# Optimization experiments

Measured on AMD Instinct MI355X. Metric: run time of the kernel, lower is better.

The kernel has to match this reference:

```python
import jax, jax.numpy as jnp
import numpy as np

EPS = 1e-5

def _bn_relu(h, gamma, beta):
    # h: (b, c, n); BatchNorm1d in training mode: stats over (batch, spatial)
    mean = jnp.mean(h, axis=(0, 2), keepdims=True)
    var = jnp.var(h, axis=(0, 2), keepdims=True)
    h = (h - mean) * jax.lax.rsqrt(var + EPS)
    h = h * gamma[None, :, None] + beta[None, :, None]
    return jax.nn.relu(h)

def setup_inputs() -> dict:
    key = jax.random.key(0)
    ks = jax.random.split(key, 8)
    b, c, n, k, N = 4, 128, 4096, 32, 16384
    x = jax.random.normal(ks[0], (b, c, n, k), dtype=jnp.float32)
    group_idx = jax.random.randint(ks[1], (b, n, k), 0, N, dtype=jnp.int64)
    fps_idx = jax.random.randint(ks[2], (b, n), 0, N, dtype=jnp.int64)
    w1 = jax.random.normal(ks[3], (c, 2 * c), dtype=jnp.float32) * (1.0 / np.sqrt(2 * c))
    b1 = jnp.zeros((c,), dtype=jnp.float32)
    g1 = jnp.ones((c,), dtype=jnp.float32)
    be1 = jnp.zeros((c,), dtype=jnp.float32)
    w2 = jax.random.normal(ks[4], (c, c), dtype=jnp.float32) * (1.0 / np.sqrt(c))
    b2 = jnp.zeros((c,), dtype=jnp.float32)
    g2 = jnp.ones((c,), dtype=jnp.float32)
    be2 = jnp.zeros((c,), dtype=jnp.float32)
    return {"x": x, "group_idx": group_idx, "fps_idx": fps_idx, "N": N,
            "w1": w1, "b1": b1, "g1": g1, "be1": be1,
            "w2": w2, "b2": b2, "g2": g2, "be2": be2}

def reference(x, group_idx, fps_idx, N, w1, b1, g1, be1, w2, b2, g2, be2):
    b, c, n, k = x.shape
    # local max pool over neighbors: (b, c, n)
    group_x = jnp.max(x, axis=-1)
    # scatter_max of (b, n*k, c) into (b, N, c), out initialized to zeros
    dil = jnp.transpose(x, (0, 2, 3, 1)).reshape(b * n * k, c)
    idx = group_idx.reshape(b, n * k) + (jnp.arange(b, dtype=group_idx.dtype) * N)[:, None]
    seg = jax.ops.segment_max(dil, idx.reshape(-1), num_segments=b * N)
    # torch scatter_max with zero-initialized out: max with 0, empty segs -> 0
    seg = jnp.maximum(seg, 0.0).reshape(b, N, c)
    # gather FPS-sampled points: (b, n, c) -> (b, c, n)
    gathered = jnp.take_along_axis(seg, fps_idx[:, :, None], axis=1)
    dilated_x = jnp.transpose(gathered, (0, 2, 1))
    feat = jnp.concatenate([group_x, dilated_x], axis=1)  # (b, 2c, n)
    h = jnp.einsum('oc,bcn->bon', w1, feat) + b1[None, :, None]
    h = _bn_relu(h, g1, be1)
    h = jnp.einsum('oc,bcn->bon', w2, h) + b2[None, :, None]
    h = _bn_relu(h, g2, be2)
    return h
```

## Files before the change

### kernel.cpp

```cpp
#include <hip/hip_runtime.h>

constexpr int Bb = 4, Cc = 128, Nn = 4096, Kk = 32, Ns = 16384;
constexpr int ROWS = Bb * Nn;
constexpr int NK = Nn * Kk;
constexpr float EPS = 1e-5f;

constexpr size_t SZ_SEG   = (size_t)Bb * Ns * Cc * 4;
constexpr size_t OFF_SEG  = 0;
constexpr size_t SZ_GX    = (size_t)ROWS * Cc * 4;
constexpr size_t OFF_GX   = OFF_SEG + SZ_SEG;
constexpr size_t OFF_H1   = OFF_GX + SZ_GX;
constexpr size_t OFF_H2   = OFF_H1 + SZ_GX;
constexpr size_t SZ_PART  = (size_t)256 * 128 * 2 * 4;
constexpr size_t OFF_P1   = OFF_H2 + SZ_GX;
constexpr size_t OFF_P2   = OFF_P1 + SZ_PART;
constexpr size_t OFF_FLAG = OFF_P2 + SZ_PART;

__global__ __launch_bounds__(256) void k_prep(const int* __restrict__ fps,
                                              float4* __restrict__ seg4,
                                              int* __restrict__ flags) {
    int i = blockIdx.x * 8 + (threadIdx.x >> 5);
    int lane = threadIdx.x & 31;
    int bb = i >> 12;
    int fi = fps[i];
    if (lane == 0) flags[bb * Ns + fi] = i;
    seg4[((size_t)bb * Ns + fi) * 32 + lane] = float4{0.f, 0.f, 0.f, 0.f};
}

__global__ __launch_bounds__(256) void k_scatter(
        const float* __restrict__ x, const int* __restrict__ gidx,
        const int* __restrict__ flags, const int* __restrict__ fps,
        float* __restrict__ gx, unsigned int* __restrict__ seg) {
    int nn = blockIdx.x, bb = blockIdx.y;
    int t = threadIdx.x;
    __shared__ float tile[128][33];
    __shared__ float gbuf[128];
    __shared__ unsigned int srow[32];
    __shared__ int klist[32];
    __shared__ int nflag;

    if (t == 0) nflag = 0;
    __syncthreads();
    if (t < 32) {
        int idxv = gidx[((bb * Nn + nn) << 5) + t];
        srow[t] = (unsigned int)(bb * Ns + idxv) * 128u;
        int fl = flags[bb * Ns + idxv];
        int j = fl & 16383;
        if (((j >> 12) == bb) && (fps[j] == idxv)) {
            int pos = atomicAdd(&nflag, 1);
            klist[pos] = t;
        }
    }

    int k4 = (t & 7) * 4;
    int cq = t >> 3;
    const float* xb = x + (size_t)bb * Cc * NK + (size_t)nn * Kk;
    float4 v[4];
    #pragma unroll
    for (int p = 0; p < 4; p++)
        v[p] = *(const float4*)(xb + (size_t)(cq + p * 32) * NK + k4);

    #pragma unroll
    for (int p = 0; p < 4; p++) {
        int ch = cq + p * 32;
        float4 w = v[p];
        float m = fmaxf(fmaxf(w.x, w.y), fmaxf(w.z, w.w));
        m = fmaxf(m, __shfl_xor(m, 1, 64));
        m = fmaxf(m, __shfl_xor(m, 2, 64));
        m = fmaxf(m, __shfl_xor(m, 4, 64));
        if ((t & 7) == 0) gbuf[ch] = m;
        tile[ch][k4 + 0] = w.x; tile[ch][k4 + 1] = w.y;
        tile[ch][k4 + 2] = w.z; tile[ch][k4 + 3] = w.w;
    }
    __syncthreads();

    int nf = nflag;
    int ch = t & 127, rep = t >> 7;
    for (int it = rep; it < nf; it += 2) {
        int k = klist[it];
        float val = tile[ch][k];
        if (val > 0.f) atomicMax(seg + srow[k] + ch, __float_as_uint(val));
    }
    if (t < 128) gx[((size_t)(bb * Nn + nn)) * 128 + t] = gbuf[t];
}

__global__ __launch_bounds__(512) void k_gemm1(
        const float* __restrict__ gx, const float* __restrict__ segf,
        const int* __restrict__ fps, const float* __restrict__ w1,
        const float* __restrict__ b1, float* __restrict__ h1,
        float* __restrict__ part) {
    __shared__ float As[32][68];
    __shared__ float Bs[32][132];
    __shared__ int rowbase[64];
    int t = threadIdx.x;
    int m0 = blockIdx.x * 64;
    if (t < 64) {
        int row = m0 + t;
        rowbase[t] = ((row >> 12) * Ns + fps[row]) * 128;
    }
    int tn = t & 31;
    int tm = t >> 5;
    float acc[4][4] = {};
    for (int k0 = 0; k0 < 256; k0 += 32) {
        __syncthreads();
        {
            int row = t >> 3;
            int c4 = (t & 7) * 4;
            int k = k0 + c4;
            float4 v;
            if (k0 < 128) v = *(const float4*)(gx + (size_t)(m0 + row) * 128 + k);
            else          v = *(const float4*)(segf + rowbase[row] + (k - 128));
            As[c4 + 0][row] = v.x; As[c4 + 1][row] = v.y;
            As[c4 + 2][row] = v.z; As[c4 + 3][row] = v.w;
        }
        #pragma unroll
        for (int i = 0; i < 2; i++) {
            int fq = t + i * 512;
            int col = fq >> 3;
            int c4 = (fq & 7) * 4;
            float4 v = *(const float4*)(w1 + (size_t)col * 256 + k0 + c4);
            Bs[c4 + 0][col] = v.x; Bs[c4 + 1][col] = v.y;
            Bs[c4 + 2][col] = v.z; Bs[c4 + 3][col] = v.w;
        }
        __syncthreads();
        #pragma unroll
        for (int kc = 0; kc < 32; kc++) {
            float4 a = *(const float4*)&As[kc][tm * 4];
            float4 bv = *(const float4*)&Bs[kc][tn * 4];
            float av[4] = {a.x, a.y, a.z, a.w};
            float bw[4] = {bv.x, bv.y, bv.z, bv.w};
            #pragma unroll
            for (int r = 0; r < 4; r++)
                #pragma unroll
                for (int c = 0; c < 4; c++) acc[r][c] += av[r] * bw[c];
        }
    }
    float4 bv = *(const float4*)(b1 + tn * 4);
    float s_[4] = {}, q_[4] = {};
    #pragma unroll
    for (int r = 0; r < 4; r++) {
        int row = m0 + tm * 4 + r;
        float o0 = acc[r][0] + bv.x, o1 = acc[r][1] + bv.y;
        float o2 = acc[r][2] + bv.z, o3 = acc[r][3] + bv.w;
        float4 o{o0, o1, o2, o3};
        *(float4*)(h1 + (size_t)row * 128 + tn * 4) = o;
        s_[0] += o0; s_[1] += o1; s_[2] += o2; s_[3] += o3;
        q_[0] += o0 * o0; q_[1] += o1 * o1; q_[2] += o2 * o2; q_[3] += o3 * o3;
    }
    __syncthreads();
    float* reds = &As[0][0];
    float* redq = &Bs[0][0];
    #pragma unroll
    for (int c = 0; c < 4; c++) {
        reds[tm * 128 + tn * 4 + c] = s_[c];
        redq[tm * 128 + tn * 4 + c] = q_[c];
    }
    __syncthreads();
    if (t < 128) {
        float s = 0.f, q = 0.f;
        #pragma unroll
        for (int j = 0; j < 16; j++) { s += reds[j * 128 + t]; q += redq[j * 128 + t]; }
        part[blockIdx.x * 128 + t] = s;
        part[32768 + blockIdx.x * 128 + t] = q;
    }
}

__global__ __launch_bounds__(512) void k_gemm2(
        const float* __restrict__ h1, const float* __restrict__ part1,
        const float* __restrict__ g1, const float* __restrict__ be1,
        const float* __restrict__ w2, const float* __restrict__ b2,
        float* __restrict__ h2, float* __restrict__ part2) {
    __shared__ float As[32][68];
    __shared__ float Bs[32][132];
    __shared__ float ssc[128], ssh[128], tmp[256];
    int t = threadIdx.x;
    int m0 = blockIdx.x * 64;
    if (t < 256) {
        int ch = t & 127;
        const float* src = part1 + (t >> 7) * 32768 + ch;
        float a = 0.f;
        #pragma unroll 8
        for (int j = 0; j < 256; j++) a += src[j * 128];
        tmp[t] = a;
    }
    __syncthreads();
    if (t < 128) {
        float mean = tmp[t] * (1.0f / 16384.0f);
        float var = tmp[t + 128] * (1.0f / 16384.0f) - mean * mean;
        float sc = g1[t] * rsqrtf(var + EPS);
        ssc[t] = sc;
        ssh[t] = be1[t] - mean * sc;
    }
    int tn = t & 31, tm = t >> 5;
    float acc[4][4] = {};
    for (int k0 = 0; k0 < 128; k0 += 32) {
        __syncthreads();
        {
            int row = t >> 3;
            int c4 = (t & 7) * 4;
            int k = k0 + c4;
            float4 v = *(const float4*)(h1 + (size_t)(m0 + row) * 128 + k);
            As[c4 + 0][row] = fmaxf(0.f, fmaf(v.x, ssc[k + 0], ssh[k + 0]));
            As[c4 + 1][row] = fmaxf(0.f, fmaf(v.y, ssc[k + 1], ssh[k + 1]));
            As[c4 + 2][row] = fmaxf(0.f, fmaf(v.z, ssc[k + 2], ssh[k + 2]));
            As[c4 + 3][row] = fmaxf(0.f, fmaf(v.w, ssc[k + 3], ssh[k + 3]));
        }
        #pragma unroll
        for (int i = 0; i < 2; i++) {
            int fq = t + i * 512;
            int col = fq >> 3;
            int c4 = (fq & 7) * 4;
            float4 v = *(const float4*)(w2 + (size_t)col * 128 + k0 + c4);
            Bs[c4 + 0][col] = v.x; Bs[c4 + 1][col] = v.y;
            Bs[c4 + 2][col] = v.z; Bs[c4 + 3][col] = v.w;
        }
        __syncthreads();
        #pragma unroll
        for (int kc = 0; kc < 32; kc++) {
            float4 a = *(const float4*)&As[kc][tm * 4];
            float4 bv = *(const float4*)&Bs[kc][tn * 4];
            float av[4] = {a.x, a.y, a.z, a.w};
            float bw[4] = {bv.x, bv.y, bv.z, bv.w};
            #pragma unroll
            for (int r = 0; r < 4; r++)
                #pragma unroll
                for (int c = 0; c < 4; c++) acc[r][c] += av[r] * bw[c];
        }
    }
    float4 bv = *(const float4*)(b2 + tn * 4);
    float s_[4] = {}, q_[4] = {};
    #pragma unroll
    for (int r = 0; r < 4; r++) {
        int row = m0 + tm * 4 + r;
        float o0 = acc[r][0] + bv.x, o1 = acc[r][1] + bv.y;
        float o2 = acc[r][2] + bv.z, o3 = acc[r][3] + bv.w;
        float4 o{o0, o1, o2, o3};
        *(float4*)(h2 + (size_t)row * 128 + tn * 4) = o;
        s_[0] += o0; s_[1] += o1; s_[2] += o2; s_[3] += o3;
        q_[0] += o0 * o0; q_[1] += o1 * o1; q_[2] += o2 * o2; q_[3] += o3 * o3;
    }
    __syncthreads();
    float* reds = &As[0][0];
    float* redq = &Bs[0][0];
    #pragma unroll
    for (int c = 0; c < 4; c++) {
        reds[tm * 128 + tn * 4 + c] = s_[c];
        redq[tm * 128 + tn * 4 + c] = q_[c];
    }
    __syncthreads();
    if (t < 128) {
        float s = 0.f, q = 0.f;
        #pragma unroll
        for (int j = 0; j < 16; j++) { s += reds[j * 128 + t]; q += redq[j * 128 + t]; }
        part2[blockIdx.x * 128 + t] = s;
        part2[32768 + blockIdx.x * 128 + t] = q;
    }
}

__global__ __launch_bounds__(512) void k_out(const float* __restrict__ h2,
                                             const float* __restrict__ part2,
                                             const float* __restrict__ g2,
                                             const float* __restrict__ be2,
                                             float* __restrict__ out) {
    __shared__ float tile[64][129];
    __shared__ float lsc[128], lsh[128], tmp[256];
    int t = threadIdx.x;
    int bb = blockIdx.y, n0 = blockIdx.x * 64;
    if (t < 256) {
        int ch = t & 127;
        const float* src = part2 + (t >> 7) * 32768 + ch;
        float a = 0.f;
        #pragma unroll 8
        for (int j = 0; j < 256; j++) a += src[j * 128];
        tmp[t] = a;
    }
    __syncthreads();
    if (t < 128) {
        float mean = tmp[t] * (1.0f / 16384.0f);
        float var = tmp[t + 128] * (1.0f / 16384.0f) - mean * mean;
        float sc = g2[t] * rsqrtf(var + EPS);
        lsc[t] = sc;
        lsh[t] = be2[t] - mean * sc;
    }
    #pragma unroll
    for (int i = 0; i < 4; i++) {
        int fq = t + i * 512;
        int row = fq >> 5;
        int c4 = (fq & 31) * 4;
        float4 v = *(const float4*)(h2 + ((size_t)(bb * Nn + n0 + row)) * 128 + c4);
        tile[row][c4 + 0] = v.x; tile[row][c4 + 1] = v.y;
        tile[row][c4 + 2] = v.z; tile[row][c4 + 3] = v.w;
    }
    __syncthreads();
    int j = t & 63, og = t >> 6;
    #pragma unroll
    for (int o = og; o < 128; o += 8) {
        float v = fmaxf(0.f, fmaf(tile[j][o], lsc[o], lsh[o]));
        out[((size_t)(bb * 128 + o)) * Nn + n0 + j] = v;
    }
}

extern "C" void kernel_launch(void* const* d_in, const int* in_sizes, int n_in,
                              void* d_out, int out_size, void* d_ws, size_t ws_size,
                              hipStream_t stream) {
    const float* x    = (const float*)d_in[0];
    const int*   gidx = (const int*)d_in[1];
    const int*   fps  = (const int*)d_in[2];
    const float* w1   = (const float*)d_in[4];
    const float* b1   = (const float*)d_in[5];
    const float* g1   = (const float*)d_in[6];
    const float* be1  = (const float*)d_in[7];
    const float* w2   = (const float*)d_in[8];
    const float* b2   = (const float*)d_in[9];
    const float* g2   = (const float*)d_in[10];
    const float* be2  = (const float*)d_in[11];
    float* out = (float*)d_out;

    char* ws = (char*)d_ws;
    unsigned int* seg  = (unsigned int*)(ws + OFF_SEG);
    float* segf        = (float*)(ws + OFF_SEG);
    float4* seg4       = (float4*)(ws + OFF_SEG);
    float* gx          = (float*)(ws + OFF_GX);
    float* h1          = (float*)(ws + OFF_H1);
    float* h2          = (float*)(ws + OFF_H2);
    float* part1       = (float*)(ws + OFF_P1);
    float* part2       = (float*)(ws + OFF_P2);
    int* flags         = (int*)(ws + OFF_FLAG);

    k_prep<<<ROWS / 8, 256, 0, stream>>>(fps, seg4, flags);
    k_scatter<<<dim3(Nn, Bb), 256, 0, stream>>>(x, gidx, flags, fps, gx, seg);
    k_gemm1<<<ROWS / 64, 512, 0, stream>>>(gx, segf, fps, w1, b1, h1, part1);
    k_gemm2<<<ROWS / 64, 512, 0, stream>>>(h1, part1, g1, be1, w2, b2, h2, part2);
    k_out<<<dim3(Nn / 64, Bb), 512, 0, stream>>>(h2, part2, g2, be2, out);
}
```

Measured before the change: 141.7 us.

## Use bf16 MFMA for both pointwise GEMMs instead of fp32 FMA

Rewrites k_gemm1 and k_gemm2 to convert the A operand and the weights to bf16 in LDS and compute with the mfma_f32_16x16x32_bf16 matrix instruction. The K step grows to 64, and the epilogue reduces per-channel sum and sum-of-squares with cross-lane shuffles. This targets the scalar FMA cost of the GEMMs, at the price of bf16 rounding error in h1, h2 and the BN statistics. The other kernels (scatter and the output stage) are unchanged, so the gain is limited to the GEMM share of total time.

```diff
diff --git a/kernel.cpp b/kernel.cpp
--- a/kernel.cpp
+++ b/kernel.cpp
@@ -4,6 +4,15 @@
 constexpr int ROWS = Bb * Nn;
 constexpr int NK = Nn * Kk;
 constexpr float EPS = 1e-5f;
+
+typedef __attribute__((ext_vector_type(8))) short short8;
+typedef __attribute__((ext_vector_type(4))) float f32x4;
+
+__device__ __forceinline__ unsigned short f2bf(float f) {
+    unsigned int u = __float_as_uint(f);
+    unsigned int r = u + 0x7FFFu + ((u >> 16) & 1u);
+    return (unsigned short)(r >> 16);
+}
 
 constexpr size_t SZ_SEG   = (size_t)Bb * Ns * Cc * 4;
 constexpr size_t OFF_SEG  = 0;
@@ -89,77 +98,69 @@
         const int* __restrict__ fps, const float* __restrict__ w1,
         const float* __restrict__ b1, float* __restrict__ h1,
         float* __restrict__ part) {
-    __shared__ float As[32][68];
-    __shared__ float Bs[32][132];
+    __shared__ __align__(16) unsigned short A_lds[64][72];
+    __shared__ __align__(16) unsigned short B_lds[128][72];
+    __shared__ float reds[4][128], redq[4][128];
     __shared__ int rowbase[64];
     int t = threadIdx.x;
     int m0 = blockIdx.x * 64;
-    if (t < 64) {
-        int row = m0 + t;
-        rowbase[t] = ((row >> 12) * Ns + fps[row]) * 128;
-    }
-    int tn = t & 31;
-    int tm = t >> 5;
-    float acc[4][4] = {};
-    for (int k0 = 0; k0 < 256; k0 += 32) {
+    if (t < 64) rowbase[t] = (((m0 + t) >> 12) * Ns + fps[m0 + t]) * 128;
+    int w = t >> 6, l = t & 63;
+    int r0 = (w >> 1) * 16, c0 = (w & 1) * 64;
+    int lr = l & 15, lk = (l >> 4) * 8;
+    f32x4 acc[4] = {};
+    for (int k0 = 0; k0 < 256; k0 += 64) {
         __syncthreads();
-        {
-            int row = t >> 3;
-            int c4 = (t & 7) * 4;
-            int k = k0 + c4;
+        #pragma unroll
+        for (int i = 0; i < 2; i++) {
+            int q = t + i * 512;
+            int row = q >> 4, kq = (q & 15) * 4;
+            int k = k0 + kq;
             float4 v;
             if (k0 < 128) v = *(const float4*)(gx + (size_t)(m0 + row) * 128 + k);
             else          v = *(const float4*)(segf + rowbase[row] + (k - 128));
-            As[c4 + 0][row] = v.x; As[c4 + 1][row] = v.y;
-            As[c4 + 2][row] = v.z; As[c4 + 3][row] = v.w;
-        }
-        #pragma unroll
-        for (int i = 0; i < 2; i++) {
-            int fq = t + i * 512;
-            int col = fq >> 3;
-            int c4 = (fq & 7) * 4;
-            float4 v = *(const float4*)(w1 + (size_t)col * 256 + k0 + c4);
-            Bs[c4 + 0][col] = v.x; Bs[c4 + 1][col] = v.y;
-            Bs[c4 + 2][col] = v.z; Bs[c4 + 3][col] = v.w;
+            ushort4 o{f2bf(v.x), f2bf(v.y), f2bf(v.z), f2bf(v.w)};
+            *(ushort4*)&A_lds[row][kq] = o;
+        }
+        #pragma unroll
+        for (int i = 0; i < 4; i++) {
+            int q = t + i * 512;
+            int col = q >> 4, kq = (q & 15) * 4;
+            float4 v = *(const float4*)(w1 + (size_t)col * 256 + k0 + kq);
+            ushort4 o{f2bf(v.x), f2bf(v.y), f2bf(v.z), f2bf(v.w)};
+            *(ushort4*)&B_lds[col][kq] = o;
         }
         __syncthreads();
         #pragma unroll
-        for (int kc = 0; kc < 32; kc++) {
-            float4 a = *(const float4*)&As[kc][tm * 4];
-            float4 bv = *(const float4*)&Bs[kc][tn * 4];
-            float av[4] = {a.x, a.y, a.z, a.w};
-            float bw[4] = {bv.x, bv.y, bv.z, bv.w};
+        for (int ks = 0; ks < 2; ks++) {
+            short8 a = *(const short8*)&A_lds[r0 + lr][ks * 32 + lk];
             #pragma unroll
-            for (int r = 0; r < 4; r++)
-                #pragma unroll
-                for (int c = 0; c < 4; c++) acc[r][c] += av[r] * bw[c];
-        }
-    }
-    float4 bv = *(const float4*)(b1 + tn * 4);
-    float s_[4] = {}, q_[4] = {};
-    #pragma unroll
-    for (int r = 0; r < 4; r++) {
-        int row = m0 + tm * 4 + r;
-        float o0 = acc[r][0] + bv.x, o1 = acc[r][1] + bv.y;
-        float o2 = acc[r][2] + bv.z, o3 = acc[r][3] + bv.w;
-        float4 o{o0, o1, o2, o3};
-        *(float4*)(h1 + (size_t)row * 128 + tn * 4) = o;
-        s_[0] += o0; s_[1] += o1; s_[2] += o2; s_[3] += o3;
-        q_[0] += o0 * o0; q_[1] += o1 * o1; q_[2] += o2 * o2; q_[3] += o3 * o3;
-    }
-    __syncthreads();
-    float* reds = &As[0][0];
-    float* redq = &Bs[0][0];
-    #pragma unroll
-    for (int c = 0; c < 4; c++) {
-        reds[tm * 128 + tn * 4 + c] = s_[c];
-        redq[tm * 128 + tn * 4 + c] = q_[c];
+            for (int cb = 0; cb < 4; cb++) {
+                short8 b = *(const short8*)&B_lds[c0 + cb * 16 + lr][ks * 32 + lk];
+                acc[cb] = __builtin_amdgcn_mfma_f32_16x16x32_bf16(a, b, acc[cb], 0, 0, 0);
+            }
+        }
+    }
+    int orow = m0 + r0 + (l >> 4) * 4;
+    #pragma unroll
+    for (int cb = 0; cb < 4; cb++) {
+        int col = c0 + cb * 16 + lr;
+        float bias = b1[col];
+        float sv = 0.f, qv = 0.f;
+        #pragma unroll
+        for (int r = 0; r < 4; r++) {
+            float o = acc[cb][r] + bias;
+            h1[(size_t)(orow + r) * 128 + col] = o;
+            sv += o; qv += o * o;
+        }
+        sv += __shfl_xor(sv, 16, 64); sv += __shfl_xor(sv, 32, 64);
+        qv += __shfl_xor(qv, 16, 64); qv += __shfl_xor(qv, 32, 64);
+        if (l < 16) { reds[w >> 1][col] = sv; redq[w >> 1][col] = qv; }
     }
     __syncthreads();
     if (t < 128) {
-        float s = 0.f, q = 0.f;
-        #pragma unroll
-        for (int j = 0; j < 16; j++) { s += reds[j * 128 + t]; q += redq[j * 128 + t]; }
+        float s = reds[0][t] + reds[1][t] + reds[2][t] + reds[3][t];
+        float q = redq[0][t] + redq[1][t] + redq[2][t] + redq[3][t];
         part[blockIdx.x * 128 + t] = s;
         part[32768 + blockIdx.x * 128 + t] = q;
     }
@@ -170,8 +171,9 @@
         const float* __restrict__ g1, const float* __restrict__ be1,
         const float* __restrict__ w2, const float* __restrict__ b2,
         float* __restrict__ h2, float* __restrict__ part2) {
-    __shared__ float As[32][68];
-    __shared__ float Bs[32][132];
+    __shared__ __align__(16) unsigned short A_lds[64][72];
+    __shared__ __align__(16) unsigned short B_lds[128][72];
+    __shared__ float reds[4][128], redq[4][128];
     __shared__ float ssc[128], ssh[128], tmp[256];
     int t = threadIdx.x;
     int m0 = blockIdx.x * 64;
@@ -191,67 +193,65 @@
         ssc[t] = sc;
         ssh[t] = be1[t] - mean * sc;
     }
-    int tn = t & 31, tm = t >> 5;
-    float acc[4][4] = {};
-    for (int k0 = 0; k0 < 128; k0 += 32) {
+    __syncthreads();
+    int w = t >> 6, l = t & 63;
+    int r0 = (w >> 1) * 16, c0 = (w & 1) * 64;
+    int lr = l & 15, lk = (l >> 4) * 8;
+    f32x4 acc[4] = {};
+    for (int k0 = 0; k0 < 128; k0 += 64) {
         __syncthreads();
-        {
-            int row = t >> 3;
-            int c4 = (t & 7) * 4;
-            int k = k0 + c4;
+        #pragma unroll
+        for (int i = 0; i < 2; i++) {
+            int q = t + i * 512;
+            int row = q >> 4, kq = (q & 15) * 4;
+            int k = k0 + kq;
             float4 v = *(const float4*)(h1 + (size_t)(m0 + row) * 128 + k);
-            As[c4 + 0][row] = fmaxf(0.f, fmaf(v.x, ssc[k + 0], ssh[k + 0]));
-            As[c4 + 1][row] = fmaxf(0.f, fmaf(v.y, ssc[k + 1], ssh[k + 1]));
-            As[c4 + 2][row] = fmaxf(0.f, fmaf(v.z, ssc[k + 2], ssh[k + 2]));
-            As[c4 + 3][row] = fmaxf(0.f, fmaf(v.w, ssc[k + 3], ssh[k + 3]));
-        }
-        #pragma unroll
-        for (int i = 0; i < 2; i++) {
-            int fq = t + i * 512;
-            int col = fq >> 3;
-            int c4 = (fq & 7) * 4;
-            float4 v = *(const float4*)(w2 + (size_t)col * 128 + k0 + c4);
-            Bs[c4 + 0][col] = v.x; Bs[c4 + 1][col] = v.y;
-            Bs[c4 + 2][col] = v.z; Bs[c4 + 3][col] = v.w;
+            float a0 = fmaxf(0.f, fmaf(v.x, ssc[k + 0], ssh[k + 0]));
+            float a1 = fmaxf(0.f, fmaf(v.y, ssc[k + 1], ssh[k + 1]));
+            float a2 = fmaxf(0.f, fmaf(v.z, ssc[k + 2], ssh[k + 2]));
+            float a3 = fmaxf(0.f, fmaf(v.w, ssc[k + 3], ssh[k + 3]));
+            ushort4 o{f2bf(a0), f2bf(a1), f2bf(a2), f2bf(a3)};
+            *(ushort4*)&A_lds[row][kq] = o;
+        }
+        #pragma unroll
+        for (int i = 0; i < 4; i++) {
+            int q = t + i * 512;
+            int col = q >> 4, kq = (q & 15) * 4;
+            float4 v = *(const float4*)(w2 + (size_t)col * 128 + k0 + kq);
+            ushort4 o{f2bf(v.x), f2bf(v.y), f2bf(v.z), f2bf(v.w)};
+            *(ushort4*)&B_lds[col][kq] = o;
         }
         __syncthreads();
         #pragma unroll
-        for (int kc = 0; kc < 32; kc++) {
-            float4 a = *(const float4*)&As[kc][tm * 4];
-            float4 bv = *(const float4*)&Bs[kc][tn * 4];
-            float av[4] = {a.x, a.y, a.z, a.w};
-            float bw[4] = {bv.x, bv.y, bv.z, bv.w};
+        for (int ks = 0; ks < 2; ks++) {
+            short8 a = *(const short8*)&A_lds[r0 + lr][ks * 32 + lk];
             #pragma unroll
-            for (int r = 0; r < 4; r++)
-                #pragma unroll
-                for (int c = 0; c < 4; c++) acc[r][c] += av[r] * bw[c];
-        }
-    }
-    float4 bv = *(const float4*)(b2 + tn * 4);
-    float s_[4] = {}, q_[4] = {};
-    #pragma unroll
-    for (int r = 0; r < 4; r++) {
-        int row = m0 + tm * 4 + r;
-        float o0 = acc[r][0] + bv.x, o1 = acc[r][1] + bv.y;
-        float o2 = acc[r][2] + bv.z, o3 = acc[r][3] + bv.w;
-        float4 o{o0, o1, o2, o3};
-        *(float4*)(h2 + (size_t)row * 128 + tn * 4) = o;
-        s_[0] += o0; s_[1] += o1; s_[2] += o2; s_[3] += o3;
-        q_[0] += o0 * o0; q_[1] += o1 * o1; q_[2] += o2 * o2; q_[3] += o3 * o3;
-    }
-    __syncthreads();
-    float* reds = &As[0][0];
-    float* redq = &Bs[0][0];
-    #pragma unroll
-    for (int c = 0; c < 4; c++) {
-        reds[tm * 128 + tn * 4 + c] = s_[c];
-        redq[tm * 128 + tn * 4 + c] = q_[c];
+            for (int cb = 0; cb < 4; cb++) {
+                short8 b = *(const short8*)&B_lds[c0 + cb * 16 + lr][ks * 32 + lk];
+                acc[cb] = __builtin_amdgcn_mfma_f32_16x16x32_bf16(a, b, acc[cb], 0, 0, 0);
+            }
+        }
+    }
+    int orow = m0 + r0 + (l >> 4) * 4;
+    #pragma unroll
+    for (int cb = 0; cb < 4; cb++) {
+        int col = c0 + cb * 16 + lr;
+        float bias = b2[col];
+        float sv = 0.f, qv = 0.f;
+        #pragma unroll
+        for (int r = 0; r < 4; r++) {
+            float o = acc[cb][r] + bias;
+            h2[(size_t)(orow + r) * 128 + col] = o;
+            sv += o; qv += o * o;
+        }
+        sv += __shfl_xor(sv, 16, 64); sv += __shfl_xor(sv, 32, 64);
+        qv += __shfl_xor(qv, 16, 64); qv += __shfl_xor(qv, 32, 64);
+        if (l < 16) { reds[w >> 1][col] = sv; redq[w >> 1][col] = qv; }
     }
     __syncthreads();
     if (t < 128) {
-        float s = 0.f, q = 0.f;
-        #pragma unroll
-        for (int j = 0; j < 16; j++) { s += reds[j * 128 + t]; q += redq[j * 128 + t]; }
+        float s = reds[0][t] + reds[1][t] + reds[2][t] + reds[3][t];
+        float q = redq[0][t] + redq[1][t] + redq[2][t] + redq[3][t];
         part2[blockIdx.x * 128 + t] = s;
         part2[32768 + blockIdx.x * 128 + t] = q;
     }
```

New measurement: 124.9 us. -11.9%, faster.
